# Optimization experiments

Measured on AMD Instinct MI355X. Metric: run time of the kernel, lower is better.

The kernel has to match this reference:

```python
import jax, jax.numpy as jnp
import numpy as np

GRID = 14  # encoded_image_size

def _grid_edge_index():
    # Exact replica of build_adjacency_matrix().nonzero(): 8-neighbor 14x14 grid.
    edges = []
    for r in range(GRID):
        for c in range(GRID):
            i = r * GRID + c
            for rr in range(max(0, r - 1), min(r + 2, GRID)):
                for cc in range(max(0, c - 1), min(c + 2, GRID)):
                    if rr == r and cc == c:
                        continue
                    edges.append((i, rr * GRID + cc))
    return np.asarray(edges, dtype=np.int64).T  # (2, 1404)


def setup_inputs() -> dict:
    key = jax.random.key(0)
    k1, k2, k3 = jax.random.split(key, 3)
    B, H, W, C, Hid = 128, 14, 14, 2048, 1024
    x = jax.random.normal(k1, (B, H, W, C), dtype=jnp.float32)
    edge_index = jnp.asarray(_grid_edge_index())
    W1 = jax.random.normal(k2, (C, Hid), dtype=jnp.float32) * (1.0 / np.sqrt(C))
    b1 = jnp.zeros((Hid,), jnp.float32)
    W2 = jax.random.normal(k3, (Hid, C), dtype=jnp.float32) * (1.0 / np.sqrt(Hid))
    b2 = jnp.zeros((C,), jnp.float32)
    return {"x": x, "edge_index": edge_index, "W1": W1, "b1": b1, "W2": W2, "b2": b2}


def _gcn_conv(h, W, b, src, dst, dinv):
    # PyG GCNConv: linear transform, symmetric deg-normalized (A+I) aggregation, bias.
    h = h @ W  # [N, out]
    norm = (dinv[src] * dinv[dst])[:, None]
    agg = jax.ops.segment_sum(h[src] * norm, dst, num_segments=h.shape[0])
    agg = agg + h * (dinv * dinv)[:, None]  # self-loop term, norm = 1/deg_i
    return agg + b


def reference(x, edge_index, W1, b1, W2, b2):
    B, H, Wd, C = x.shape
    N = B * H * Wd
    # Faithful to original: permute(0,3,1,2) then reshape(-1, C) (layout-scrambling).
    xf = jnp.transpose(x, (0, 3, 1, 2)).reshape(-1, C)  # [N, C]
    src, dst = edge_index[0], edge_index[1]
    # Degrees over ALL N nodes: self-loop (=1) everywhere + incoming grid edges
    # (only first 196 nodes have grid neighbors; rest are passthrough).
    deg = jnp.ones((N,), xf.dtype).at[dst].add(1.0)
    dinv = jax.lax.rsqrt(deg)
    h = jax.nn.relu(_gcn_conv(xf, W1, b1, src, dst, dinv))
    h = jax.nn.relu(_gcn_conv(h, W2, b2, src, dst, dinv))
    # reshape + permute(0,3,1,2) + permute(0,2,3,1) == identity back to NHWC.
    return h.reshape(B, H, Wd, C)
```

## Files before the change

kernel.cpp:

```cpp
#include <hip/hip_runtime.h>

typedef float  float4_t __attribute__((ext_vector_type(4)));
typedef __bf16 bf16x8   __attribute__((ext_vector_type(8)));

#define BM 256
#define BN 256
#define BK 64

#define GLD16(g, l)                                                        \
    __builtin_amdgcn_global_load_lds(                                      \
        (const __attribute__((address_space(1))) void*)(g),                \
        (__attribute__((address_space(3))) void*)(l), 16, 0, 0)

__global__ __launch_bounds__(256)
void transpose_x_kernel(const float* __restrict__ x, __bf16* __restrict__ A1)
{
    __shared__ float sm[32 * 221];
    const int b  = blockIdx.y;
    const int c0 = blockIdx.x * 32;
    const int t  = threadIdx.x;

    const float* xb = x + (size_t)b * 401408;
    const int c4 = (t & 7) * 4;
    const int p0 = t >> 3;
#pragma unroll
    for (int k = 0; k < 7; ++k) {
        int p = p0 + k * 32;
        if (p < 196) {
            float4_t v = *(const float4_t*)&xb[(size_t)p * 2048 + c0 + c4];
#pragma unroll
            for (int i = 0; i < 4; ++i)
                sm[(c4 + i) * 221 + p + (p >> 3)] = v[i];
        }
    }
    __syncthreads();

    __bf16* ab = A1 + (size_t)b * 401408 + (size_t)c0 * 196;
#pragma unroll
    for (int k = 0; k < 4; ++k) {
        int o8 = k * 256 + t;
        if (o8 < 784) {
            int o  = o8 * 8;
            int cc = o / 196;
            int pp = o - cc * 196;
            bf16x8 v;
#pragma unroll
            for (int i = 0; i < 8; ++i) {
                v[i] = (__bf16)sm[cc * 221 + pp + (pp >> 3)];
                if (++pp == 196) { pp = 0; ++cc; }
            }
            *(bf16x8*)(ab + o) = v;
        }
    }
}

__global__ void transpose_w_kernel(const float* __restrict__ W, __bf16* __restrict__ Wt,
                                   int K, int N)
{
    __shared__ float tile[32][33];
    const int kt = blockIdx.x * 32, nt = blockIdx.y * 32;
    const int tx = threadIdx.x, ty = threadIdx.y;
#pragma unroll
    for (int rr = 0; rr < 4; ++rr)
        tile[ty + rr * 8][tx] = W[(size_t)(kt + ty + rr * 8) * N + nt + tx];
    __syncthreads();
#pragma unroll
    for (int rr = 0; rr < 4; ++rr)
        Wt[(size_t)(nt + ty + rr * 8) * K + kt + tx] = (__bf16)tile[tx][ty + rr * 8];
}

template<bool OUT_BF16, int LNX>
__global__ __launch_bounds__(512, 2)
void gemm_bt_kernel(const __bf16* __restrict__ A,
                    const __bf16* __restrict__ Bt,
                    const float* __restrict__ bias,
                    void* __restrict__ out,
                    float* __restrict__ raw_out,
                    int M, int N, int K)
{
    __shared__ __bf16 lds[2 * 32768];

    const int tid  = threadIdx.x;
    const int wid  = tid >> 6;
    const int lane = tid & 63;

    const int lid  = blockIdx.x + gridDim.x * blockIdx.y;
    const int xcd  = lid & 7;
    const int i0   = lid >> 3;
    const int ni   = i0 & ((1 << LNX) - 1);
    const int mseq = i0 >> LNX;
    const int mi   = (mseq << 3) + xcd;
    const int row0 = mi * BM;
    if (row0 >= M) return;
    const int col0 = ni * BN;

    const int wave_m = (wid >> 2) * 128;
    const int wave_n = (wid & 3) * 64;

    float4_t acc[8][4];
#pragma unroll
    for (int i = 0; i < 8; ++i)
#pragma unroll
        for (int j = 0; j < 4; ++j)
            acc[i][j] = (float4_t){0.f, 0.f, 0.f, 0.f};

    const int    srow = (wid << 3) + (lane >> 3);
    const int    scol = ((lane & 7) ^ (lane >> 3)) << 3;
    const int    wdst = wid << 9;
    const __bf16* gA  = A  + (size_t)(row0 + srow) * K + scol;
    const __bf16* gB  = Bt + (size_t)(col0 + srow) * K + scol;

#define AS(s, ko, d) GLD16(gA + (size_t)(s) * 64 * K + (ko), (d) + (s) * 4096 + wdst)
#define BS(s, ko, d) GLD16(gB + (size_t)(s) * 64 * K + (ko), (d) + 16384 + (s) * 4096 + wdst)

    AS(0, 0, lds); AS(1, 0, lds); AS(2, 0, lds); AS(3, 0, lds);
    BS(0, 0, lds); BS(1, 0, lds); BS(2, 0, lds); BS(3, 0, lds);
    asm volatile("s_waitcnt vmcnt(0)" ::: "memory");
    __builtin_amdgcn_s_barrier();
    __builtin_amdgcn_sched_barrier(0);

    const int m15  = lane & 15;
    const int q    = lane >> 4;
    const int l7   = lane & 7;
    const int swz0 = ((q) ^ l7) << 3;
    const int swz1 = ((4 + q) ^ l7) << 3;
    const int arow = (wave_m + m15) * 64;
    const int brow = 16384 + (wave_n + m15) * 64;

#define PHASE_SYNC()                                            \
    __builtin_amdgcn_s_barrier();                               \
    asm volatile("s_waitcnt lgkmcnt(0)" ::: "memory");          \
    __builtin_amdgcn_sched_barrier(0)

    const int NTt = K >> 6;
    for (int kt = 0; kt < NTt; ++kt) {
        const __bf16* cA  = lds + (kt & 1) * 32768;
        __bf16*       dst = lds + ((kt + 1) & 1) * 32768;
        const bool    st  = (kt < NTt - 1);
        const size_t  ko  = (size_t)(kt + 1) * 64;

        bf16x8 bfr[4], afA[4], afB[4];

#pragma unroll
        for (int j = 0; j < 4; ++j) bfr[j] = *(const bf16x8*)&cA[brow + j * 1024 + swz0];
#pragma unroll
        for (int i = 0; i < 4; ++i) afA[i] = *(const bf16x8*)&cA[arow + i * 1024 + swz0];
        if (st) { AS(0, ko, dst); AS(1, ko, dst); AS(2, ko, dst); }
        PHASE_SYNC();
        __builtin_amdgcn_s_setprio(1);
#pragma unroll
        for (int i = 0; i < 4; ++i)
#pragma unroll
            for (int j = 0; j < 4; ++j)
                acc[i][j] = __builtin_amdgcn_mfma_f32_16x16x32_bf16(
                    afA[i], bfr[j], acc[i][j], 0, 0, 0);
        __builtin_amdgcn_s_setprio(0);
        __builtin_amdgcn_s_barrier();

#pragma unroll
        for (int i = 0; i < 4; ++i) afB[i] = *(const bf16x8*)&cA[arow + (i + 4) * 1024 + swz0];
        if (st) { AS(3, ko, dst); BS(0, ko, dst); BS(1, ko, dst); }
        PHASE_SYNC();
        __builtin_amdgcn_s_setprio(1);
#pragma unroll
        for (int i = 0; i < 4; ++i)
#pragma unroll
            for (int j = 0; j < 4; ++j)
                acc[i + 4][j] = __builtin_amdgcn_mfma_f32_16x16x32_bf16(
                    afB[i], bfr[j], acc[i + 4][j], 0, 0, 0);
        __builtin_amdgcn_s_setprio(0);
        __builtin_amdgcn_s_barrier();

#pragma unroll
        for (int j = 0; j < 4; ++j) bfr[j] = *(const bf16x8*)&cA[brow + j * 1024 + swz1];
#pragma unroll
        for (int i = 0; i < 4; ++i) afA[i] = *(const bf16x8*)&cA[arow + i * 1024 + swz1];
        if (st) { BS(2, ko, dst); BS(3, ko, dst); }
        PHASE_SYNC();
        __builtin_amdgcn_s_setprio(1);
#pragma unroll
        for (int i = 0; i < 4; ++i)
#pragma unroll
            for (int j = 0; j < 4; ++j)
                acc[i][j] = __builtin_amdgcn_mfma_f32_16x16x32_bf16(
                    afA[i], bfr[j], acc[i][j], 0, 0, 0);
        __builtin_amdgcn_s_setprio(0);
        __builtin_amdgcn_s_barrier();

#pragma unroll
        for (int i = 0; i < 4; ++i) afB[i] = *(const bf16x8*)&cA[arow + (i + 4) * 1024 + swz1];
        PHASE_SYNC();
        __builtin_amdgcn_s_setprio(1);
#pragma unroll
        for (int i = 0; i < 4; ++i)
#pragma unroll
            for (int j = 0; j < 4; ++j)
                acc[i + 4][j] = __builtin_amdgcn_mfma_f32_16x16x32_bf16(
                    afB[i], bfr[j], acc[i + 4][j], 0, 0, 0);
        __builtin_amdgcn_s_setprio(0);
        __builtin_amdgcn_sched_barrier(0);
        if (st) asm volatile("s_waitcnt vmcnt(0)" ::: "memory");
        __builtin_amdgcn_s_barrier();
        __builtin_amdgcn_sched_barrier(0);
    }
#undef AS
#undef BS
#undef PHASE_SYNC

    const int crow = (lane >> 4) * 4;
    const int ccol = lane & 15;
    const bool has_raw = (row0 == 0);
#pragma unroll
    for (int i = 0; i < 8; ++i) {
#pragma unroll
        for (int j = 0; j < 4; ++j) {
            int gcol = col0 + wave_n + j * 16 + ccol;
            float bv = bias[gcol];
#pragma unroll
            for (int r = 0; r < 4; ++r) {
                int grow = row0 + wave_m + i * 16 + crow + r;
                float v = acc[i][j][r];
                if (has_raw && grow < 196) raw_out[grow * N + gcol] = v;
                float o = fmaxf(v + bv, 0.f);
                if (OUT_BF16) ((__bf16*)out)[(size_t)grow * N + gcol] = (__bf16)o;
                else          ((float*)out)[(size_t)grow * N + gcol] = o;
            }
        }
    }
}

template<typename OutT>
__global__ void fixup_kernel(const float* __restrict__ raw, const float* __restrict__ bias,
                             OutT* __restrict__ out, int N)
{
    const int q = blockIdx.x;
    const int r = q / 14, c = q % 14;
    int nbr[8];
    int cnt = 0;
    for (int rr = (r > 0 ? r - 1 : 0); rr <= (r < 13 ? r + 1 : 13); ++rr)
        for (int cc = (c > 0 ? c - 1 : 0); cc <= (c < 13 ? c + 1 : 13); ++cc)
            if (!(rr == r && cc == c)) nbr[cnt++] = rr * 14 + cc;
    const float dq    = 1.f / sqrtf(1.f + (float)cnt);
    const float wself = 1.f / (1.f + (float)cnt);
    float wn[8];
    for (int t = 0; t < cnt; ++t) {
        int pr = nbr[t] / 14, pc = nbr[t] % 14;
        int pcnt = ((pr < 13 ? pr + 1 : 13) - (pr > 0 ? pr - 1 : 0) + 1) *
                   ((pc < 13 ? pc + 1 : 13) - (pc > 0 ? pc - 1 : 0) + 1) - 1;
        wn[t] = dq / sqrtf(1.f + (float)pcnt);
    }
    const int ch = blockIdx.y * 256 + threadIdx.x;
    float s = raw[q * N + ch] * wself;
    for (int t = 0; t < cnt; ++t) s += raw[nbr[t] * N + ch] * wn[t];
    float o = fmaxf(s + bias[ch], 0.f);
    out[(size_t)q * N + ch] = (OutT)o;
}

extern "C" void kernel_launch(void* const* d_in, const int* in_sizes, int n_in,
                              void* d_out, int out_size, void* d_ws, size_t ws_size,
                              hipStream_t stream)
{
    const float* x  = (const float*)d_in[0];
    const float* W1 = (const float*)d_in[2];
    const float* b1 = (const float*)d_in[3];
    const float* W2 = (const float*)d_in[4];
    const float* b2 = (const float*)d_in[5];

    const int M = 25088, C = 2048, Hid = 1024;

    __bf16* A1 = (__bf16*)d_out;

    char* ws = (char*)d_ws;
    __bf16* A2    = (__bf16*)(ws);
    __bf16* W1t   = (__bf16*)(ws + 51380224);
    __bf16* W2t   = (__bf16*)(ws + 55574528);
    float*  h1raw = (float*)(ws + 59768832);
    float*  h2raw = (float*)(ws + 60571648);

    transpose_x_kernel<<<dim3(64, 128), 256, 0, stream>>>(x, A1);
    transpose_w_kernel<<<dim3(C / 32, Hid / 32), dim3(32, 8), 0, stream>>>(W1, W1t, C, Hid);
    transpose_w_kernel<<<dim3(Hid / 32, C / 32), dim3(32, 8), 0, stream>>>(W2, W2t, Hid, C);

    gemm_bt_kernel<true, 2><<<dim3(Hid / BN, 104), 512, 0, stream>>>(
        A1, W1t, b1, (void*)A2, h1raw, M, Hid, C);
    fixup_kernel<__bf16><<<dim3(196, Hid / 256), 256, 0, stream>>>(h1raw, b1, A2, Hid);

    gemm_bt_kernel<false, 3><<<dim3(C / BN, 104), 512, 0, stream>>>(
        A2, W2t, b2, d_out, h2raw, M, C, Hid);
    fixup_kernel<float><<<dim3(196, C / 256), 256, 0, stream>>>(h2raw, b2, (float*)d_out, C);
}
```

Baseline: 629.9 us.

## Switch GEMM to BK=32 with four-stage LDS ring and three tiles in flight

The bf16 GEMM main loop moves from a double-buffered BK=64 pipeline to a 4-slot LDS ring of BK=32 tiles, with three K-tiles of global-to-LDS loads in flight at once. Partial vmcnt waits replace the full drain each iteration. The staging layout and swizzle are reworked to match the smaller tile. The goal is to hide global memory latency better at the same LDS footprint, at the cost of twice as many loop iterations and barriers per K and a more fragile swizzle and waitcnt accounting.

```diff
diff --git a/kernel.cpp b/kernel.cpp
--- a/kernel.cpp
+++ b/kernel.cpp
@@ -5,7 +5,7 @@
 
 #define BM 256
 #define BN 256
-#define BK 64
+#define BK 32
 
 #define GLD16(g, l)                                                        \
     __builtin_amdgcn_global_load_lds(                                      \
@@ -78,7 +78,7 @@
                     float* __restrict__ raw_out,
                     int M, int N, int K)
 {
-    __shared__ __bf16 lds[2 * 32768];
+    __shared__ __bf16 lds[4 * 16384];
 
     const int tid  = threadIdx.x;
     const int wid  = tid >> 6;
@@ -104,48 +104,47 @@
         for (int j = 0; j < 4; ++j)
             acc[i][j] = (float4_t){0.f, 0.f, 0.f, 0.f};
 
-    const int    srow = (wid << 3) + (lane >> 3);
-    const int    scol = ((lane & 7) ^ (lane >> 3)) << 3;
-    const int    wdst = wid << 9;
-    const __bf16* gA  = A  + (size_t)(row0 + srow) * K + scol;
-    const __bf16* gB  = Bt + (size_t)(col0 + srow) * K + scol;
-
-#define AS(s, ko, d) GLD16(gA + (size_t)(s) * 64 * K + (ko), (d) + (s) * 4096 + wdst)
-#define BS(s, ko, d) GLD16(gB + (size_t)(s) * 64 * K + (ko), (d) + 16384 + (s) * 4096 + wdst)
-
-    AS(0, 0, lds); AS(1, 0, lds); AS(2, 0, lds); AS(3, 0, lds);
-    BS(0, 0, lds); BS(1, 0, lds); BS(2, 0, lds); BS(3, 0, lds);
-    asm volatile("s_waitcnt vmcnt(0)" ::: "memory");
+    const int    stg_row = (wid << 4) + ((lane >> 3) << 1) + ((lane >> 2) & 1);
+    const int    stg_k   = (((lane & 3) ^ ((lane >> 3) & 3)) << 3);
+    const int    wdst    = wid << 9;
+    const __bf16* gA     = A  + (size_t)(row0 + stg_row) * K + stg_k;
+    const __bf16* gB     = Bt + (size_t)(col0 + stg_row) * K + stg_k;
+
+#define AS(s, ko, d) GLD16(gA + (size_t)(s) * 128 * K + (ko), (d) + (s) * 4096 + wdst)
+#define BS(s, ko, d) GLD16(gB + (size_t)(s) * 128 * K + (ko), (d) + 8192 + (s) * 4096 + wdst)
+
+    AS(0, 0, lds);      AS(1, 0, lds);      BS(0, 0, lds);      BS(1, 0, lds);
+    AS(0, 32, lds + 16384); AS(1, 32, lds + 16384); BS(0, 32, lds + 16384); BS(1, 32, lds + 16384);
+    AS(0, 64, lds + 32768); AS(1, 64, lds + 32768); BS(0, 64, lds + 32768); BS(1, 64, lds + 32768);
+    asm volatile("s_waitcnt vmcnt(8)" ::: "memory");
     __builtin_amdgcn_s_barrier();
     __builtin_amdgcn_sched_barrier(0);
 
-    const int m15  = lane & 15;
-    const int q    = lane >> 4;
-    const int l7   = lane & 7;
-    const int swz0 = ((q) ^ l7) << 3;
-    const int swz1 = ((4 + q) ^ l7) << 3;
-    const int arow = (wave_m + m15) * 64;
-    const int brow = 16384 + (wave_n + m15) * 64;
+    const int m15   = lane & 15;
+    const int slotf = ((lane & 1) << 2) + ((lane >> 4) ^ ((lane >> 1) & 3));
+    const int la_base = ((wave_m >> 1) + (m15 >> 1)) * 64 + slotf * 8;
+    const int lb_base = 8192 + ((wave_n >> 1) + (m15 >> 1)) * 64 + slotf * 8;
 
 #define PHASE_SYNC()                                            \
     __builtin_amdgcn_s_barrier();                               \
     asm volatile("s_waitcnt lgkmcnt(0)" ::: "memory");          \
     __builtin_amdgcn_sched_barrier(0)
 
-    const int NTt = K >> 6;
-    for (int kt = 0; kt < NTt; ++kt) {
-        const __bf16* cA  = lds + (kt & 1) * 32768;
-        __bf16*       dst = lds + ((kt + 1) & 1) * 32768;
-        const bool    st  = (kt < NTt - 1);
-        const size_t  ko  = (size_t)(kt + 1) * 64;
+    const int NTt = K >> 5;
+    int cur = 0, st3 = 3;
+    for (int t = 0; t < NTt; ++t) {
+        const __bf16* cA  = lds + cur * 16384;
+        __bf16*       dst = lds + st3 * 16384;
+        const bool    st  = (t < NTt - 3);
+        const size_t  ko  = (size_t)(t + 3) * 32;
 
         bf16x8 bfr[4], afA[4], afB[4];
 
 #pragma unroll
-        for (int j = 0; j < 4; ++j) bfr[j] = *(const bf16x8*)&cA[brow + j * 1024 + swz0];
-#pragma unroll
-        for (int i = 0; i < 4; ++i) afA[i] = *(const bf16x8*)&cA[arow + i * 1024 + swz0];
-        if (st) { AS(0, ko, dst); AS(1, ko, dst); AS(2, ko, dst); }
+        for (int j = 0; j < 4; ++j) bfr[j] = *(const bf16x8*)&cA[lb_base + j * 512];
+#pragma unroll
+        for (int i = 0; i < 4; ++i) afA[i] = *(const bf16x8*)&cA[la_base + i * 512];
+        if (st) { AS(0, ko, dst); AS(1, ko, dst); }
         PHASE_SYNC();
         __builtin_amdgcn_s_setprio(1);
 #pragma unroll
@@ -158,37 +157,8 @@
         __builtin_amdgcn_s_barrier();
 
 #pragma unroll
-        for (int i = 0; i < 4; ++i) afB[i] = *(const bf16x8*)&cA[arow + (i + 4) * 1024 + swz0];
-        if (st) { AS(3, ko, dst); BS(0, ko, dst); BS(1, ko, dst); }
-        PHASE_SYNC();
-        __builtin_amdgcn_s_setprio(1);
-#pragma unroll
-        for (int i = 0; i < 4; ++i)
-#pragma unroll
-            for (int j = 0; j < 4; ++j)
-                acc[i + 4][j] = __builtin_amdgcn_mfma_f32_16x16x32_bf16(
-                    afB[i], bfr[j], acc[i + 4][j], 0, 0, 0);
-        __builtin_amdgcn_s_setprio(0);
-        __builtin_amdgcn_s_barrier();
-
-#pragma unroll
-        for (int j = 0; j < 4; ++j) bfr[j] = *(const bf16x8*)&cA[brow + j * 1024 + swz1];
-#pragma unroll
-        for (int i = 0; i < 4; ++i) afA[i] = *(const bf16x8*)&cA[arow + i * 1024 + swz1];
-        if (st) { BS(2, ko, dst); BS(3, ko, dst); }
-        PHASE_SYNC();
-        __builtin_amdgcn_s_setprio(1);
-#pragma unroll
-        for (int i = 0; i < 4; ++i)
-#pragma unroll
-            for (int j = 0; j < 4; ++j)
-                acc[i][j] = __builtin_amdgcn_mfma_f32_16x16x32_bf16(
-                    afA[i], bfr[j], acc[i][j], 0, 0, 0);
-        __builtin_amdgcn_s_setprio(0);
-        __builtin_amdgcn_s_barrier();
-
-#pragma unroll
-        for (int i = 0; i < 4; ++i) afB[i] = *(const bf16x8*)&cA[arow + (i + 4) * 1024 + swz1];
+        for (int i = 0; i < 4; ++i) afB[i] = *(const bf16x8*)&cA[la_base + (i + 4) * 512];
+        if (st) { BS(0, ko, dst); BS(1, ko, dst); }
         PHASE_SYNC();
         __builtin_amdgcn_s_setprio(1);
 #pragma unroll
@@ -199,9 +169,14 @@
                     afB[i], bfr[j], acc[i + 4][j], 0, 0, 0);
         __builtin_amdgcn_s_setprio(0);
         __builtin_amdgcn_sched_barrier(0);
-        if (st) asm volatile("s_waitcnt vmcnt(0)" ::: "memory");
+        if (t < NTt - 3)       asm volatile("s_waitcnt vmcnt(8)" ::: "memory");
+        else if (t == NTt - 3) asm volatile("s_waitcnt vmcnt(4)" ::: "memory");
+        else if (t == NTt - 2) asm volatile("s_waitcnt vmcnt(0)" ::: "memory");
         __builtin_amdgcn_s_barrier();
         __builtin_amdgcn_sched_barrier(0);
+
+        cur = (cur + 1) & 3;
+        st3 = (st3 + 1) & 3;
     }
 #undef AS
 #undef BS
```

Measured after the change: 650.0 us. 3.2% more time.
